# Performance work log

Measured on AMD Instinct MI355X. Metric: run time of the kernel, lower is better.

The kernel has to match this reference:

```python
import jax, jax.numpy as jnp
import numpy as np

N = 100000   # nodes
F = 128      # feature dim (== numEdges ctor arg)
H = 64       # hidden_dim
E = 1600000  # edges (avg degree 16)


def setup_inputs() -> dict:
    key = jax.random.key(0)
    ks = jax.random.split(key, 8)
    x = jax.random.normal(ks[0], (N, F), dtype=jnp.float32)
    edge_index = jax.random.randint(ks[1], (2, E), 0, N)
    sF = 1.0 / np.sqrt(F)
    sH = 1.0 / np.sqrt(H)
    conv_W = jax.random.normal(ks[2], (F, F), dtype=jnp.float32) * sF  # GCNConv linear weight
    conv_b = jnp.zeros((F,), dtype=jnp.float32)
    w1 = jax.random.normal(ks[3], (H, F), dtype=jnp.float32) * sF
    b1 = jnp.zeros((H,), dtype=jnp.float32)
    w2 = jax.random.normal(ks[4], (H, H), dtype=jnp.float32) * sH
    b2 = jnp.zeros((H,), dtype=jnp.float32)
    w3 = jax.random.normal(ks[5], (1, H), dtype=jnp.float32) * sH
    b3 = jnp.zeros((1,), dtype=jnp.float32)
    return dict(x=x, edge_index=edge_index, conv_W=conv_W, conv_b=conv_b,
                w1=w1, b1=b1, w2=w2, b2=b2, w3=w3, b3=b3)


def reference(x, edge_index, conv_W, conv_b, w1, b1, w2, b2, w3, b3):
    n = x.shape[0]
    # --- GCNConv: D^{-1/2}(A+I)D^{-1/2} X W + b ---
    xw = x @ conv_W.T                                   # [N, F]
    loops = jnp.arange(n)
    src = jnp.concatenate([edge_index[0], loops])       # add self-loops
    dst = jnp.concatenate([edge_index[1], loops])
    deg = jax.ops.segment_sum(jnp.ones(src.shape[0], xw.dtype), dst, num_segments=n)
    dinv = jnp.where(deg > 0, jax.lax.rsqrt(deg), 0.0)
    norm = dinv[src] * dinv[dst]                        # [E+N]
    h = jax.ops.segment_sum(xw[src] * norm[:, None], dst, num_segments=n) + conv_b  # [N, F]
    # --- MedianAggregation (index=None -> single segment, 'lower' interpolation) ---
    med = jnp.sort(h, axis=0)[(n - 1) // 2][None, :]    # [1, F]
    # --- tanh MLP ---
    a = jnp.tanh(med @ w1.T + b1)
    a = jnp.tanh(a @ w2.T + b2)
    return a @ w3.T + b3                                # [1, 1]
```

## Files before the change

kernel.cpp:

```cpp
#include <hip/hip_runtime.h>
#include <math.h>


#define CAP    24576
#define NREG   8
#define RCAP   3072
#define MPT    24
#define CCAP   96
#define CSTR   97
#define DSTR   32
#define OVCAP  4096
#define SPCAP  2048
#define BCAP   4608
#define NBKMAX 400
#define CH     4096

typedef __attribute__((ext_vector_type(8))) short short8;
typedef __attribute__((ext_vector_type(4))) float f32x4;
typedef __attribute__((ext_vector_type(8))) _Float16 half8;
typedef __attribute__((ext_vector_type(2))) _Float16 half2v;

__device__ __forceinline__ unsigned ordKey(float x) {
    unsigned u = __float_as_uint(x);
    return (u & 0x80000000u) ? ~u : (u | 0x80000000u);
}
__device__ __forceinline__ unsigned short f2bf(float f) {
    unsigned u = __float_as_uint(f);
    return (unsigned short)((u + 0x7FFFu + ((u >> 16) & 1u)) >> 16);
}

__global__ void k_init(int* __restrict__ cursor, int* __restrict__ below8,
                       int* __restrict__ candCnt8, int* __restrict__ ovCnt,
                       const float* __restrict__ W, short* __restrict__ Whi,
                       short* __restrict__ Wlo, int nbk) {
    if (blockIdx.x == 1) {
        for (int idx = threadIdx.x; idx < 16384; idx += 256) {
            int j = idx & 7, lane = (idx >> 3) & 63;
            int t = (idx >> 9) & 7, s = idx >> 12;
            int row = t * 16 + (lane & 15);
            int k = s * 32 + (lane >> 4) * 8 + j;
            float w = W[row * 128 + k];
            unsigned short hb = f2bf(w);
            float hf = __uint_as_float((unsigned)hb << 16);
            Whi[idx] = (short)hb;
            Wlo[idx] = (short)f2bf(w - hf);
        }
        return;
    }
    int t = threadIdx.x;
    for (int i = t; i < nbk; i += 256) cursor[i] = 0;
    for (int i = t; i < NREG * 128; i += 256) { below8[i] = 0; candCnt8[i] = 0; }
    if (t == 0) { ovCnt[0] = 0; ovCnt[1] = 0; ovCnt[2] = 0; }
}

__global__ __launch_bounds__(256) void k_binGemm(
        const float* __restrict__ x, const short* __restrict__ Whi,
        const short* __restrict__ Wlo, _Float16* __restrict__ xw, int n, int GB,
        const int* __restrict__ src, const int* __restrict__ dst, int E,
        int* __restrict__ cursor, int2* __restrict__ binned,
        int* __restrict__ ovCnt, int2* __restrict__ ovBuf, int nbk) {
    __shared__ char smem[40960];
    const int t = threadIdx.x;
    if ((int)blockIdx.x < GB) {
        float* trn = (float*)smem;
        const int lane = t & 63, wv = t >> 6;
        const int quad = lane >> 4, m = lane & 15;
        const int rowBase = blockIdx.x * 64 + wv * 16;
        const int r = rowBase + m;
        const int rl = r < n ? r : (n - 1);
        f32x4 acc[8];
        #pragma unroll
        for (int q = 0; q < 8; q++) acc[q] = (f32x4){0.f, 0.f, 0.f, 0.f};
        #pragma unroll
        for (int s = 0; s < 4; s++) {
            const float* xp = x + (size_t)rl * 128 + s * 32 + quad * 8;
            float4 p0 = *(const float4*)xp;
            float4 p1 = *(const float4*)(xp + 4);
            float f[8] = {p0.x, p0.y, p0.z, p0.w, p1.x, p1.y, p1.z, p1.w};
            short8 ah, al;
            #pragma unroll
            for (int j = 0; j < 8; j++) {
                unsigned short hb = f2bf(f[j]);
                float hf = __uint_as_float((unsigned)hb << 16);
                ah[j] = (short)hb;
                al[j] = (short)f2bf(f[j] - hf);
            }
            #pragma unroll
            for (int q = 0; q < 8; q++) {
                short8 bh = *(const short8*)(Whi + (((s * 8 + q) * 64 + lane) << 3));
                short8 bl = *(const short8*)(Wlo + (((s * 8 + q) * 64 + lane) << 3));
                acc[q] = __builtin_amdgcn_mfma_f32_16x16x32_bf16(ah, bh, acc[q], 0, 0, 0);
                acc[q] = __builtin_amdgcn_mfma_f32_16x16x32_bf16(al, bh, acc[q], 0, 0, 0);
                acc[q] = __builtin_amdgcn_mfma_f32_16x16x32_bf16(ah, bl, acc[q], 0, 0, 0);
            }
        }
        float* tw = trn + wv * (16 * 132);
        #pragma unroll
        for (int q = 0; q < 8; q++)
            #pragma unroll
            for (int e = 0; e < 4; e++)
                tw[(quad * 4 + e) * 132 + q * 16 + m] = acc[q][e];
        #pragma unroll
        for (int i = 0; i < 4; i++) {
            int row = i * 4 + (lane >> 4);
            int c8 = lane & 15;
            const float* tp = tw + row * 132 + c8 * 8;
            float4 p0 = *(const float4*)tp;
            float4 p1 = *(const float4*)(tp + 4);
            half8 o;
            o[0] = (_Float16)p0.x; o[1] = (_Float16)p0.y;
            o[2] = (_Float16)p0.z; o[3] = (_Float16)p0.w;
            o[4] = (_Float16)p1.x; o[5] = (_Float16)p1.y;
            o[6] = (_Float16)p1.z; o[7] = (_Float16)p1.w;
            int grow = rowBase + row;
            if (grow < n) *(half8*)(xw + (size_t)grow * 128 + c8 * 8) = o;
        }
    } else {
        int2* sorted = (int2*)smem;
        int* hist  = (int*)(smem + 32768);
        int* gbase = hist + NBKMAX;
        int* lpre  = gbase + NBKMAX;
        int* hist2 = lpre + NBKMAX;
        int* sbase = hist2 + NBKMAX;
        int* wscan = sbase + NBKMAX;
        const int e0 = ((int)blockIdx.x - GB) * CH;
        const int len = min(CH, E - e0);
        for (int i = t; i < nbk; i += 256) { hist[i] = 0; hist2[i] = 0; }
        __syncthreads();
        for (int k = t; k < len; k += 256)
            atomicAdd(&hist[dst[e0 + k] >> 8], 1);
        __syncthreads();
        for (int i = t; i < nbk; i += 256) {
            int c = hist[i];
            if (c) {
                int g = atomicAdd(&cursor[i], c);
                if (g + c <= BCAP) gbase[i] = g;
                else {
                    gbase[i] = -1;
                    sbase[i] = atomicAdd(ovCnt, c);
                }
            }
        }
        {
            const int i0 = t * 2, i1 = i0 + 1;
            int h0 = (i0 < nbk) ? hist[i0] : 0;
            int h1 = (i1 < nbk) ? hist[i1] : 0;
            int s = h0 + h1;
            const int lane = t & 63, wv = t >> 6;
            int sc = s;
            #pragma unroll
            for (int off = 1; off < 64; off <<= 1) {
                int y = __shfl_up(sc, off, 64);
                if (lane >= off) sc += y;
            }
            if (lane == 63) wscan[wv] = sc;
            __syncthreads();
            int wbase = 0;
            for (int ww = 0; ww < wv; ww++) wbase += wscan[ww];
            int excl = wbase + sc - s;
            if (i0 < nbk) lpre[i0] = excl;
            if (i1 < nbk) lpre[i1] = excl + h0;
        }
        __syncthreads();
        for (int k = t; k < len; k += 256) {
            int s = src[e0 + k], d = dst[e0 + k];
            int b = d >> 8;
            int p = atomicAdd(&hist2[b], 1);
            sorted[lpre[b] + p] = make_int2(s, d);
        }
        __syncthreads();
        for (int k = t; k < len; k += 256) {
            int2 e = sorted[k];
            int b = e.y >> 8;
            int li = k - lpre[b];
            int g = gbase[b];
            if (g >= 0) binned[(size_t)b * BCAP + g + li] = e;
            else {
                int o = sbase[b] + li;
                if (o < OVCAP) ovBuf[o] = make_int2(e.y, e.x);
            }
        }
    }
}

__global__ __launch_bounds__(1024) void k_build(int2* __restrict__ binned,
                                                const int* __restrict__ cursor,
                                                float* __restrict__ dinv,
                                                unsigned char* __restrict__ deg8,
                                                int* __restrict__ ovCnt,
                                                int2* __restrict__ ovBuf,
                                                int* __restrict__ spillNodes, int n) {
    __shared__ int ladj[256 * DSTR];
    __shared__ int lcnt[256];
    const int b = blockIdx.x, t = threadIdx.x;
    const int cnt = min(cursor[b], BCAP);
    const size_t e0 = (size_t)b * BCAP;
    if (t < 256) lcnt[t] = 0;
    __syncthreads();
    for (int k = t; k < cnt; k += 1024) {
        int2 e = binned[e0 + k];
        int li = e.y & 255;
        int pos = atomicAdd(&lcnt[li], 1);
        if (pos < DSTR) ladj[li * DSTR + pos] = e.x;
        else {
            int o = atomicAdd(ovCnt, 1);
            if (o < OVCAP) ovBuf[o] = make_int2(e.y, e.x);
        }
    }
    __syncthreads();
    int4* adjOut = (int4*)((int*)binned + e0 * 2);
    const int4* lsrc4 = (const int4*)ladj;
    for (int i = t; i < 2048; i += 1024) adjOut[i] = lsrc4[i];
    if (t < 256) {
        int node = b * 256 + t;
        if (node < n) {
            int deg = lcnt[t];
            dinv[node] = (float)(1.0 / sqrt((double)(deg + 1)));
            deg8[node] = (unsigned char)(deg < 255 ? deg : 255);
            if (deg > DSTR) {
                int p = atomicAdd(ovCnt + 1, 1);
                if (p < SPCAP) spillNodes[p] = node;
            }
        }
    }
}

__global__ __launch_bounds__(256) void k_aggH(const _Float16* __restrict__ xw,
                                              const unsigned char* __restrict__ deg8,
                                              const int* __restrict__ adjAll,
                                              const float* __restrict__ dinv,
                                              const float* __restrict__ conv_b,
                                              _Float16* __restrict__ h, int n) {
    const int d = blockIdx.x * 4 + (threadIdx.x >> 6);
    if (d >= n) return;
    const int lane = threadIdx.x & 63;
    const int l32 = lane & 31;
    const int grp = lane >> 4, sub = lane & 15;
    int degT = deg8[d];
    const int degB = degT < DSTR ? degT : DSTR;
    const float dd = dinv[d];
    const int* adjRow = adjAll + (size_t)(d >> 8) * (BCAP * 2) + (d & 255) * DSTR;
    int aj = adjRow[l32];
    bool ev = (lane < 32) && (l32 < degB);
    int ajs = ev ? aj : 0;
    float dv = ev ? dinv[ajs] : 0.f;
    const half8* xw8 = (const half8*)xw;
    float acc[8];
    if (grp == 0) {
        half8 a = xw8[(unsigned)(d * 16 + sub)];
        const float w0 = dd * dd;
        #pragma unroll
        for (int e = 0; e < 8; e++) acc[e] = w0 * (float)a[e];
    } else {
        #pragma unroll
        for (int e = 0; e < 8; e++) acc[e] = 0.f;
    }
    for (int j = 0; j < degB; j += 4) {
        const int jj = j + grp;
        bool ok = jj < degB;
        int sv = __shfl(ajs, jj, 64);
        float w = dd * __shfl(dv, jj, 64);
        int so = ok ? sv : 0;
        w = ok ? w : 0.f;
        half8 v = xw8[(unsigned)(so * 16 + sub)];
        #pragma unroll
        for (int e = 0; e < 8; e++) acc[e] += w * (float)v[e];
    }
    #pragma unroll
    for (int e = 0; e < 8; e++) {
        acc[e] += __shfl_xor(acc[e], 16, 64);
        acc[e] += __shfl_xor(acc[e], 32, 64);
    }
    if (lane < 16) {
        const float4* cb4 = (const float4*)(conv_b + sub * 8);
        float4 c0 = cb4[0], c1 = cb4[1];
        float cb[8] = {c0.x, c0.y, c0.z, c0.w, c1.x, c1.y, c1.z, c1.w};
        half8 o;
        #pragma unroll
        for (int e = 0; e < 8; e++) o[e] = (_Float16)(acc[e] + cb[e]);
        ((half8*)h)[(unsigned)(d * 16 + sub)] = o;
    }
}

__global__ __launch_bounds__(1024) void k_sampleSpill(
        _Float16* h, int n,
        unsigned* __restrict__ Lkey, unsigned* __restrict__ Ukey,
        const _Float16* __restrict__ xw, const int* __restrict__ spillNodes,
        const int* __restrict__ adjAll, const float* __restrict__ dinv,
        const float* __restrict__ conv_b, const int2* __restrict__ ovBuf,
        const int* __restrict__ ovCnt) {
    const int t = threadIdx.x;
    if (blockIdx.x >= 128) {
        int m = ovCnt[0];  if (m > OVCAP) m = OVCAP;
        int sp = ovCnt[1]; if (sp > SPCAP) sp = SPCAP;
        if (t >= 128) return;
        for (int i = (int)blockIdx.x - 128; i < sp; i += 16) {
            const int d = spillNodes[i];
            const float dd = dinv[d];
            float acc = dd * dd * (float)xw[(size_t)d * 128 + t];
            const int* adjRow = adjAll + (size_t)(d >> 8) * (BCAP * 2) + (d & 255) * DSTR;
            for (int j = 0; j < DSTR; j++) {
                int a = adjRow[j];
                acc += dd * dinv[a] * (float)xw[(size_t)a * 128 + t];
            }
            for (int k = 0; k < m; k++) {
                int2 e = ovBuf[k];
                if (e.x == d)
                    acc += dd * dinv[e.y] * (float)xw[(size_t)e.y * 128 + t];
            }
            h[(size_t)d * 128 + t] = (_Float16)(acc + conv_b[t]);
        }
        return;
    }
    __shared__ int hist[2048];
    __shared__ int wsum[4];
    const int c = blockIdx.x;
    for (int i = t; i < 2048; i += 1024) hist[i] = 0;
    __syncthreads();
    const int ns = (n + 31) >> 5;
    for (int i = t; i < ns; i += 1024) {
        float v = (float)h[(size_t)(i << 5) * 128 + c];
        atomicAdd(&hist[ordKey(v) >> 21], 1);
    }
    __syncthreads();
    int ps = 0, sc = 0;
    const int lane = t & 63, wv = t >> 6;
    if (t < 256) {
        #pragma unroll
        for (int b = 0; b < 8; b++) ps += hist[t * 8 + b];
        sc = ps;
        #pragma unroll
        for (int off = 1; off < 64; off <<= 1) {
            int y = __shfl_up(sc, off, 64);
            if (lane >= off) sc += y;
        }
        if (lane == 63) wsum[wv] = sc;
    }
    __syncthreads();
    if (t < 256) {
        int wbase = 0;
        for (int ww = 0; ww < wv; ww++) wbase += wsum[ww];
        const int excl = wbase + sc - ps;
        const int sMid = (ns - 1) >> 1;
        const int delta = (int)(4.0f * sqrtf((float)ns)) + 1;
        int sLo = sMid - delta; if (sLo < 0) sLo = 0;
        int sHi = sMid + delta; if (sHi > ns - 1) sHi = ns - 1;
        if (sLo >= excl && sLo < excl + ps) {
            int rem = sLo - excl, b = t * 8;
            for (;; b++) { int cc = hist[b]; if (rem < cc) break; rem -= cc; }
            Lkey[c] = (unsigned)b << 21;
        }
        if (sHi >= excl && sHi < excl + ps) {
            int rem = sHi - excl, b = t * 8;
            for (;; b++) { int cc = hist[b]; if (rem < cc) break; rem -= cc; }
            Ukey[c] = (((unsigned)(b + 1)) << 21) - 1u;
        }
    }
}

__global__ __launch_bounds__(256) void k_classify(const _Float16* __restrict__ h,
                                                  int total8,
                                                  const unsigned* __restrict__ Lkey,
                                                  const unsigned* __restrict__ Ukey,
                                                  int* __restrict__ below8,
                                                  int* __restrict__ candCnt8,
                                                  _Float16* __restrict__ cand) {
    __shared__ _Float16 buf[128 * CSTR];
    __shared__ int cN[128], cB[128];
    const int t = threadIdx.x;
    const int rid = (int)blockIdx.x & (NREG - 1);
    for (int i = t; i < 128; i += 256) { cN[i] = 0; cB[i] = 0; }
    __syncthreads();
    const int stride = gridDim.x * blockDim.x;
    const int i0 = blockIdx.x * blockDim.x + t;
    const int jb = (i0 << 3) & 127;
    unsigned L[8], U[8];
    #pragma unroll
    for (int k = 0; k < 8; k++) { L[k] = Lkey[jb + k]; U[k] = Ukey[jb + k]; }
    int b[8] = {0, 0, 0, 0, 0, 0, 0, 0};
    const half8* hv = (const half8*)h;
    for (int i = i0; i < total8; i += stride) {
        half8 v = hv[i];
        #pragma unroll
        for (int k = 0; k < 8; k++) {
            float f = (float)v[k];
            unsigned u = ordKey(f);
            if (u < L[k]) b[k]++;
            else if (u <= U[k]) {
                int p = atomicAdd(&cN[jb + k], 1);
                if (p < CCAP) buf[(jb + k) * CSTR + p] = v[k];
                else {
                    int g = atomicAdd(&candCnt8[rid * 128 + jb + k], 1);
                    if (g < RCAP)
                        cand[(size_t)(jb + k) * CAP + rid * RCAP + g] = v[k];
                }
            }
        }
    }
    #pragma unroll
    for (int k = 0; k < 8; k++)
        if (b[k]) atomicAdd(&cB[jb + k], b[k]);
    __syncthreads();
    if (t < 128) {
        if (cB[t]) atomicAdd(&below8[rid * 128 + t], cB[t]);
        int nn = cN[t] < CCAP ? cN[t] : CCAP;
        if (nn) {
            int base = atomicAdd(&candCnt8[rid * 128 + t], nn);
            for (int k2 = 0; k2 < nn && base + k2 < RCAP; k2++)
                cand[(size_t)t * CAP + rid * RCAP + base + k2] = buf[t * CSTR + k2];
        }
    }
}

__global__ __launch_bounds__(1024) void k_finalMlp(
        const _Float16* __restrict__ cand, const int* __restrict__ candCnt8,
        const int* __restrict__ below8, int n, float* __restrict__ med,
        int* __restrict__ doneCnt,
        const float* __restrict__ w1, const float* __restrict__ b1,
        const float* __restrict__ w2, const float* __restrict__ b2,
        const float* __restrict__ w3, const float* __restrict__ b3,
        float* __restrict__ out) {
    __shared__ int wsum[16];
    __shared__ int lastFlag;
    const int c = blockIdx.x, t = threadIdx.x;
    const int lane = t & 63, wv = t >> 6;
    int below_tot = 0;
    #pragma unroll
    for (int rr = 0; rr < NREG; rr++) below_tot += below8[rr * 128 + c];
    int cnt = 0;
    unsigned short myk[MPT];
    const unsigned short* cbase = (const unsigned short*)cand + (size_t)c * CAP;
    #pragma unroll
    for (int rr = 0; rr < NREG; rr++) {
        int cr = candCnt8[rr * 128 + c]; if (cr > RCAP) cr = RCAP;
        cnt += cr;
        const unsigned short* rp = cbase + rr * RCAP;
        #pragma unroll
        for (int k = 0; k < RCAP / 1024; k++) {
            int i = t + k * 1024;
            unsigned ub = (i < cr) ? (unsigned)rp[i] : 0u;
            unsigned kk = (ub & 0x8000u) ? (~ub & 0xFFFFu) : (ub | 0x8000u);
            myk[rr * (RCAP / 1024) + k] =
                (i < cr) ? (unsigned short)kk : (unsigned short)0xFFFFu;
        }
    }
    int r = (n - 1) / 2 - below_tot;
    if (r < 0) r = 0;
    if (r >= cnt) r = cnt - 1;
    unsigned cur = 0;
    for (int bit = 15; bit >= 0; bit--) {
        const unsigned pivot = cur | (1u << bit);
        int lc = 0;
        #pragma unroll
        for (int mi = 0; mi < MPT; mi++) lc += ((unsigned)myk[mi] < pivot) ? 1 : 0;
        #pragma unroll
        for (int off = 32; off > 0; off >>= 1) lc += __shfl_down(lc, off, 64);
        if (lane == 0) wsum[wv] = lc;
        __syncthreads();
        int tot = 0;
        #pragma unroll
        for (int ww = 0; ww < 16; ww++) tot += wsum[ww];
        if (tot <= r) cur = pivot;
        __syncthreads();
    }
    if (t == 0) {
        unsigned short bits = (cur & 0x8000u) ? (unsigned short)(cur & 0x7FFFu)
                                              : (unsigned short)(~cur & 0xFFFFu);
        _Float16 hv;
        *(unsigned short*)&hv = bits;
        med[c] = (float)hv;
        __threadfence();
        int old = atomicAdd(doneCnt, 1);
        lastFlag = (old == 127);
    }
    __syncthreads();
    if (!lastFlag) return;
    __threadfence();
    __shared__ float m[128], a1[64], a2[64];
    if (t < 128) m[t] = med[t];
    __syncthreads();
    if (t < 64) {
        float acc = b1[t];
        for (int f = 0; f < 128; f++) acc += m[f] * w1[t * 128 + f];
        a1[t] = tanhf(acc);
    }
    __syncthreads();
    if (t < 64) {
        float acc = b2[t];
        for (int f = 0; f < 64; f++) acc += a1[f] * w2[t * 64 + f];
        a2[t] = tanhf(acc);
    }
    __syncthreads();
    if (t == 0) {
        float acc = b3[0];
        for (int f = 0; f < 64; f++) acc += a2[f] * w3[f];
        out[0] = acc;
    }
}

extern "C" void kernel_launch(void* const* d_in, const int* in_sizes, int n_in,
                              void* d_out, int out_size, void* d_ws, size_t ws_size,
                              hipStream_t stream) {
    const float* x      = (const float*)d_in[0];
    const int*   ei     = (const int*)d_in[1];
    const float* conv_W = (const float*)d_in[2];
    const float* conv_b = (const float*)d_in[3];
    const float* w1 = (const float*)d_in[4];
    const float* b1 = (const float*)d_in[5];
    const float* w2 = (const float*)d_in[6];
    const float* b2 = (const float*)d_in[7];
    const float* w3 = (const float*)d_in[8];
    const float* b3 = (const float*)d_in[9];

    const int N = in_sizes[0] / 128;
    const int E = in_sizes[1] / 2;
    const int* src = ei;
    const int* dst = ei + E;
    const int NBK = (N + 255) / 256;

    char* p = (char*)d_ws;
    auto alloc = [&](size_t bytes) -> char* {
        char* q = p;
        p += (bytes + 255) & ~(size_t)255;
        return q;
    };
    _Float16* xw  = (_Float16*)alloc((size_t)N * 128 * 2);
    _Float16* h   = (_Float16*)alloc((size_t)N * 128 * 2);
    int2*  binned = (int2*)alloc((size_t)NBK * BCAP * 8);
    _Float16* cand = (_Float16*)alloc((size_t)128 * CAP * 2);
    float* dinv   = (float*)alloc((size_t)N * 4);
    unsigned char* deg8 = (unsigned char*)alloc((size_t)N);
    int*   cursor = (int*)alloc((size_t)NBK * 4);
    short* Whi    = (short*)alloc(16384 * 2);
    short* Wlo    = (short*)alloc(16384 * 2);
    int2*  ovBuf  = (int2*)alloc((size_t)OVCAP * 8);
    int*   ovCnt  = (int*)alloc(256);
    int*   spillNodes = (int*)alloc((size_t)SPCAP * 4);
    unsigned* Lkey = (unsigned*)alloc(128 * 4);
    unsigned* Ukey = (unsigned*)alloc(128 * 4);
    int*   below8   = (int*)alloc((size_t)NREG * 128 * 4);
    int*   candCnt8 = (int*)alloc((size_t)NREG * 128 * 4);
    float* med     = (float*)alloc(128 * 4);

    const int GB   = (N + 63) / 64;
    const int BINB = (E + CH - 1) / CH;

    k_init<<<2, 256, 0, stream>>>(cursor, below8, candCnt8, ovCnt, conv_W,
                                  Whi, Wlo, NBK);
    k_binGemm<<<GB + BINB, 256, 0, stream>>>(x, Whi, Wlo, xw, N, GB,
                                             src, dst, E, cursor, binned,
                                             ovCnt, ovBuf, NBK);
    k_build<<<NBK, 1024, 0, stream>>>(binned, cursor, dinv, deg8, ovCnt, ovBuf,
                                      spillNodes, N);
    k_aggH<<<(N + 3) / 4, 256, 0, stream>>>(xw, deg8, (const int*)binned, dinv,
                                            conv_b, h, N);
    k_sampleSpill<<<144, 1024, 0, stream>>>(h, N, Lkey, Ukey, xw, spillNodes,
                                            (const int*)binned, dinv, conv_b,
                                            ovBuf, ovCnt);
    k_classify<<<512, 256, 0, stream>>>(h, N * 16, Lkey, Ukey, below8, candCnt8,
                                        cand);
    k_finalMlp<<<128, 1024, 0, stream>>>(cand, candCnt8, below8, N, med,
                                         ovCnt + 2, w1, b1, w2, b2, w3, b3,
                                         (float*)d_out);
}
```

Before: 285.6 us.

## Split aggregation feature halves across XCC groups for L2 locality

```diff
diff --git a/kernel.cpp b/kernel.cpp
--- a/kernel.cpp
+++ b/kernel.cpp
@@ -32,7 +32,8 @@
 __global__ void k_init(int* __restrict__ cursor, int* __restrict__ below8,
                        int* __restrict__ candCnt8, int* __restrict__ ovCnt,
                        const float* __restrict__ W, short* __restrict__ Whi,
-                       short* __restrict__ Wlo, int nbk) {
+                       short* __restrict__ Wlo, int nbk,
+                       int* __restrict__ pairFlag, int npair) {
     if (blockIdx.x == 1) {
         for (int idx = threadIdx.x; idx < 16384; idx += 256) {
             int j = idx & 7, lane = (idx >> 3) & 63;
@@ -50,6 +51,7 @@
     int t = threadIdx.x;
     for (int i = t; i < nbk; i += 256) cursor[i] = 0;
     for (int i = t; i < NREG * 128; i += 256) { below8[i] = 0; candCnt8[i] = 0; }
+    for (int i = t; i < npair; i += 256) pairFlag[i] = 0;
     if (t == 0) { ovCnt[0] = 0; ovCnt[1] = 0; ovCnt[2] = 0; }
 }
 
@@ -230,24 +232,39 @@
                                               const int* __restrict__ adjAll,
                                               const float* __restrict__ dinv,
                                               const float* __restrict__ conv_b,
-                                              _Float16* __restrict__ h, int n) {
-    const int d = blockIdx.x * 4 + (threadIdx.x >> 6);
-    if (d >= n) return;
-    const int lane = threadIdx.x & 63;
-    const int l32 = lane & 31;
-    const int grp = lane >> 4, sub = lane & 15;
-    int degT = deg8[d];
-    const int degB = degT < DSTR ? degT : DSTR;
-    const float dd = dinv[d];
-    const int* adjRow = adjAll + (size_t)(d >> 8) * (BCAP * 2) + (d & 255) * DSTR;
+                                              _Float16* __restrict__ hout, int n,
+                                              int* __restrict__ pairFlag) {
+    __shared__ int sHalf;
+    const int b = blockIdx.x;
+    const int p = b >> 1;
+    if (threadIdx.x == 0) {
+        unsigned xcc = 0;
+        asm volatile("s_getreg_b32 %0, hwreg(HW_REG_XCC_ID)" : "=s"(xcc));
+        int pref = (int)((xcc >> 2) & 1u);
+        int old = atomicCAS(&pairFlag[p], 0, pref + 1);
+        sHalf = (old == 0) ? pref : (2 - old);
+    }
+    __syncthreads();
+    const int hf = sHalf;
+    const int t = threadIdx.x;
+    const int lane = t & 63, wv = t >> 6;
+    const int nd = lane >> 5, l32 = lane & 31;
+    const int grp = l32 >> 3, s8 = l32 & 7;
+    const int d = p * 8 + wv * 2 + nd;
+    const bool valid = d < n;
+    const int dl = valid ? d : (n - 1);
+    int myDeg = deg8[dl]; if (myDeg > DSTR) myDeg = DSTR;
+    const float dd = dinv[dl];
+    const int* adjRow = adjAll + (size_t)(dl >> 8) * (BCAP * 2) + (dl & 255) * DSTR;
     int aj = adjRow[l32];
-    bool ev = (lane < 32) && (l32 < degB);
+    bool ev = l32 < myDeg;
     int ajs = ev ? aj : 0;
     float dv = ev ? dinv[ajs] : 0.f;
     const half8* xw8 = (const half8*)xw;
+    const unsigned rowOff = (unsigned)hf * 8 + (unsigned)s8;
     float acc[8];
     if (grp == 0) {
-        half8 a = xw8[(unsigned)(d * 16 + sub)];
+        half8 a = xw8[(unsigned)dl * 16 + rowOff];
         const float w0 = dd * dd;
         #pragma unroll
         for (int e = 0; e < 8; e++) acc[e] = w0 * (float)a[e];
@@ -255,30 +272,30 @@
         #pragma unroll
         for (int e = 0; e < 8; e++) acc[e] = 0.f;
     }
-    for (int j = 0; j < degB; j += 4) {
+    for (int j = 0; j < myDeg; j += 4) {
         const int jj = j + grp;
-        bool ok = jj < degB;
-        int sv = __shfl(ajs, jj, 64);
-        float w = dd * __shfl(dv, jj, 64);
+        bool ok = jj < myDeg;
+        int sv = __shfl(ajs, jj, 32);
+        float w = dd * __shfl(dv, jj, 32);
         int so = ok ? sv : 0;
         w = ok ? w : 0.f;
-        half8 v = xw8[(unsigned)(so * 16 + sub)];
+        half8 v = xw8[(unsigned)so * 16 + rowOff];
         #pragma unroll
         for (int e = 0; e < 8; e++) acc[e] += w * (float)v[e];
     }
     #pragma unroll
     for (int e = 0; e < 8; e++) {
+        acc[e] += __shfl_xor(acc[e], 8, 64);
         acc[e] += __shfl_xor(acc[e], 16, 64);
-        acc[e] += __shfl_xor(acc[e], 32, 64);
-    }
-    if (lane < 16) {
-        const float4* cb4 = (const float4*)(conv_b + sub * 8);
+    }
+    if (grp == 0 && valid) {
+        const float4* cb4 = (const float4*)(conv_b + hf * 64 + s8 * 8);
         float4 c0 = cb4[0], c1 = cb4[1];
         float cb[8] = {c0.x, c0.y, c0.z, c0.w, c1.x, c1.y, c1.z, c1.w};
         half8 o;
         #pragma unroll
         for (int e = 0; e < 8; e++) o[e] = (_Float16)(acc[e] + cb[e]);
-        ((half8*)h)[(unsigned)(d * 16 + sub)] = o;
+        ((half8*)hout)[(unsigned)d * 16 + rowOff] = o;
     }
 }
 
@@ -517,6 +534,7 @@
     const int* src = ei;
     const int* dst = ei + E;
     const int NBK = (N + 255) / 256;
+    const int NPAIR = (N + 7) / 8;
 
     char* p = (char*)d_ws;
     auto alloc = [&](size_t bytes) -> char* {
@@ -536,6 +554,7 @@
     int2*  ovBuf  = (int2*)alloc((size_t)OVCAP * 8);
     int*   ovCnt  = (int*)alloc(256);
     int*   spillNodes = (int*)alloc((size_t)SPCAP * 4);
+    int*   pairFlag = (int*)alloc((size_t)NPAIR * 4);
     unsigned* Lkey = (unsigned*)alloc(128 * 4);
     unsigned* Ukey = (unsigned*)alloc(128 * 4);
     int*   below8   = (int*)alloc((size_t)NREG * 128 * 4);
@@ -546,14 +565,14 @@
     const int BINB = (E + CH - 1) / CH;
 
     k_init<<<2, 256, 0, stream>>>(cursor, below8, candCnt8, ovCnt, conv_W,
-                                  Whi, Wlo, NBK);
+                                  Whi, Wlo, NBK, pairFlag, NPAIR);
     k_binGemm<<<GB + BINB, 256, 0, stream>>>(x, Whi, Wlo, xw, N, GB,
                                              src, dst, E, cursor, binned,
                                              ovCnt, ovBuf, NBK);
     k_build<<<NBK, 1024, 0, stream>>>(binned, cursor, dinv, deg8, ovCnt, ovBuf,
                                       spillNodes, N);
-    k_aggH<<<(N + 3) / 4, 256, 0, stream>>>(xw, deg8, (const int*)binned, dinv,
-                                            conv_b, h, N);
+    k_aggH<<<NPAIR * 2, 256, 0, stream>>>(xw, deg8, (const int*)binned, dinv,
+                                          conv_b, h, N, pairFlag);
     k_sampleSpill<<<144, 1024, 0, stream>>>(h, N, Lkey, Ukey, xw, spillNodes,
                                             (const int*)binned, dinv, conv_b,
                                             ovBuf, ovCnt);
```

Measured after the change: 288.9 us. About the same (+1.2%).
